# Kernel tuning notes

Hardware: AMD Instinct MI355X
Metric: run time of the kernel (lower is better)

Reference implementation:

```python
import jax, jax.numpy as jnp
import numpy as np

N_NODES = 50000
N_EDGES = 800000
N_FEAT = 256
HIDDEN = 64
N_CLASSES = 16
T_END = 3.0  # opt['time']; rk4 takes one step over [0, 3]


def spline_conv(x, src, dst, p, W, R, b, n):
    """SplineConv, dim=1, kernel_size=2, degree=1 open B-spline, aggr='mean'.
    x: [n, Cin]; src/dst: [E]; p: [E,1] pseudo-coords in [0,1];
    W: [2, Cin, Cout]; R: [Cin, Cout]; b: [Cout]."""
    xj = x[src]  # gather source node features [E, Cin]
    # basis weights for K=2, degree=1: (1-p) on kernel 0, p on kernel 1
    msg = ((1.0 - p) * xj) @ W[0] + (p * xj) @ W[1]  # [E, Cout]
    agg = jax.ops.segment_sum(msg, dst, num_segments=n)
    deg = jax.ops.segment_sum(jnp.ones((msg.shape[0], 1), msg.dtype), dst, num_segments=n)
    return agg / jnp.maximum(deg, 1.0) + x @ R + b


def setup_inputs() -> dict:
    key = jax.random.key(0)
    ks = jax.random.split(key, 20)
    x = jax.random.normal(ks[0], (N_NODES, N_FEAT), jnp.float32)
    edge_attr = jax.random.uniform(ks[1], (N_EDGES, 1), jnp.float32)
    src = jax.random.randint(ks[2], (N_EDGES,), 0, N_NODES)
    dst = jax.random.randint(ks[3], (N_EDGES,), 0, N_NODES)

    def w(k, shape, fan_in):
        s = 1.0 / np.sqrt(fan_in)
        return jax.random.uniform(k, shape, jnp.float32, -s, s)

    # conv1: num_features -> hidden
    W1 = w(ks[4], (2, N_FEAT, HIDDEN), N_FEAT)
    R1 = w(ks[5], (N_FEAT, HIDDEN), N_FEAT)
    b1 = jnp.zeros((HIDDEN,), jnp.float32)
    # ODE func: two stacked SplineConvs hidden -> hidden
    Wa = w(ks[6], (2, HIDDEN, HIDDEN), HIDDEN)
    Ra = w(ks[7], (HIDDEN, HIDDEN), HIDDEN)
    ba = jnp.zeros((HIDDEN,), jnp.float32)
    Wb = w(ks[8], (2, HIDDEN, HIDDEN), HIDDEN)
    Rb = w(ks[9], (HIDDEN, HIDDEN), HIDDEN)
    bb = jnp.zeros((HIDDEN,), jnp.float32)
    # conv2: hidden -> num_classes
    W2 = w(ks[10], (2, HIDDEN, N_CLASSES), HIDDEN)
    R2 = w(ks[11], (HIDDEN, N_CLASSES), HIDDEN)
    b2 = jnp.zeros((N_CLASSES,), jnp.float32)

    return dict(x=x, edge_attr=edge_attr, src=src, dst=dst,
                W1=W1, R1=R1, b1=b1, Wa=Wa, Ra=Ra, ba=ba,
                Wb=Wb, Rb=Rb, bb=bb, W2=W2, R2=R2, b2=b2)


def reference(x, edge_attr, src, dst, W1, R1, b1, Wa, Ra, ba, Wb, Rb, bb, W2, R2, b2):
    n = x.shape[0]
    p = edge_attr
    h = jnp.tanh(spline_conv(x, src, dst, p, W1, R1, b1, n))
    # dropout is identity in eval mode

    def f(y):  # GCNLayer: two stacked SplineConvs, no activation
        y = spline_conv(y, src, dst, p, Wa, Ra, ba, n)
        return spline_conv(y, src, dst, p, Wb, Rb, bb, n)

    # single RK4 step from t=0 to t=T_END (torchdiffeq fixed-grid rk4 on s_span=[0,3])
    k1 = f(h)
    k2 = f(h + 0.5 * T_END * k1)
    k3 = f(h + 0.5 * T_END * k2)
    k4 = f(h + T_END * k3)
    h = h + (T_END / 6.0) * (k1 + 2.0 * k2 + 2.0 * k3 + k4)

    out = jnp.tanh(spline_conv(h, src, dst, p, W2, R2, b2, n))
    return jax.nn.log_softmax(out, axis=1)
```

## Files before the change

### kernel.cpp

```cpp
#include <hip/hip_runtime.h>
#include <math.h>

static inline int ceil_div(int a, int b) { return (a + b - 1) / b; }


__global__ __launch_bounds__(256) void setup_zero_pack(
    int* __restrict__ deg, int* __restrict__ fill, int n,
    const float* __restrict__ W1, const float* __restrict__ R1,
    const float* __restrict__ Wa, const float* __restrict__ Ra,
    const float* __restrict__ Wb, const float* __restrict__ Rb,
    const float* __restrict__ W2, const float* __restrict__ R2,
    float* __restrict__ Bc1, float* __restrict__ Bca,
    float* __restrict__ Bcb, float* __restrict__ Bc2) {
    int gid = blockIdx.x * 256 + threadIdx.x;
    int gstride = gridDim.x * 256;
    for (int i = gid; i < n; i += gstride) { deg[i] = 0; fill[i] = 0; }
    const int S1 = 256 * 192, S2 = 192 * 64, S4 = 64 * 48;
    const int TOT = S1 + 2 * S2 + S4;
    for (int i0 = gid; i0 < TOT; i0 += gstride) {
        int idx = i0;
        if (idx < S1) {
            int k = idx / 192, c = idx % 192;
            float v;
            if (c < 64)       v = W1[k * 64 + c];
            else if (c < 128) v = W1[256 * 64 + k * 64 + (c - 64)];
            else              v = R1[k * 64 + (c - 128)];
            Bc1[idx] = v;
            continue;
        }
        idx -= S1;
        if (idx < S2) { Bca[idx] = (idx < 8192) ? Wa[idx] : Ra[idx - 8192]; continue; }
        idx -= S2;
        if (idx < S2) { Bcb[idx] = (idx < 8192) ? Wb[idx] : Rb[idx - 8192]; continue; }
        idx -= S2;
        int k = idx / 48, c = idx % 48;
        float v;
        if (c < 16)      v = W2[k * 16 + c];
        else if (c < 32) v = W2[64 * 16 + k * 16 + (c - 16)];
        else             v = R2[k * 16 + (c - 32)];
        Bc2[idx] = v;
    }
}

__global__ __launch_bounds__(256) void hist_kernel(const int* __restrict__ dst,
                                                   int* __restrict__ deg, int E) {
    int e = blockIdx.x * 256 + threadIdx.x;
    if (e < E) atomicAdd(&deg[dst[e]], 1);
}

__global__ __launch_bounds__(256) void scan_blocksum(const int* __restrict__ deg,
                                                     int* __restrict__ bsum, int n) {
    __shared__ int red[256];
    int t = threadIdx.x;
    int base = blockIdx.x * 2048 + t * 8;
    int s = 0;
    #pragma unroll
    for (int i = 0; i < 8; ++i) {
        int idx = base + i;
        if (idx < n) s += deg[idx];
    }
    red[t] = s;
    __syncthreads();
    #pragma unroll
    for (int off = 128; off >= 1; off >>= 1) {
        if (t < off) red[t] += red[t + off];
        __syncthreads();
    }
    if (t == 0) bsum[blockIdx.x] = red[0];
}

__global__ __launch_bounds__(256) void scan_tops(int* __restrict__ bsum, int nb) {
    __shared__ int sh[256];
    int t = threadIdx.x;
    int orig = (t < nb) ? bsum[t] : 0;
    sh[t] = orig;
    __syncthreads();
    for (int off = 1; off < 256; off <<= 1) {
        int add = (t >= off) ? sh[t - off] : 0;
        __syncthreads();
        sh[t] += add;
        __syncthreads();
    }
    if (t < nb) bsum[t] = sh[t] - orig;
}

__global__ __launch_bounds__(256) void scan_final(const int* __restrict__ deg,
                                                  const int* __restrict__ bsum,
                                                  int* __restrict__ rowp,
                                                  float* __restrict__ invd,
                                                  int n, int E) {
    __shared__ int sh[256];
    int t = threadIdx.x;
    int base = blockIdx.x * 2048 + t * 8;
    int loc[8];
    int s = 0;
    #pragma unroll
    for (int i = 0; i < 8; ++i) {
        int idx = base + i;
        int d = (idx < n) ? deg[idx] : 0;
        loc[i] = d;
        s += d;
    }
    sh[t] = s;
    __syncthreads();
    for (int off = 1; off < 256; off <<= 1) {
        int add = (t >= off) ? sh[t - off] : 0;
        __syncthreads();
        sh[t] += add;
        __syncthreads();
    }
    int run = bsum[blockIdx.x] + (sh[t] - s);
    #pragma unroll
    for (int i = 0; i < 8; ++i) {
        int idx = base + i;
        if (idx < n) {
            rowp[idx] = run;
            int d = loc[i];
            run += d;
            invd[idx] = 1.0f / (float)(d > 1 ? d : 1);
        }
    }
    if (blockIdx.x == 0 && t == 0) rowp[n] = E;
}

__global__ __launch_bounds__(256) void scatter_idx(const int* __restrict__ dst,
                                                   const int* __restrict__ rowp,
                                                   int* __restrict__ fill,
                                                   int* __restrict__ ei, int E) {
    int e = blockIdx.x * 256 + threadIdx.x;
    if (e >= E) return;
    int d = dst[e];
    int pos = rowp[d] + atomicAdd(&fill[d], 1);
    ei[pos] = e;
}

__global__ __launch_bounds__(256) void sort_fill(const int* __restrict__ rowp,
                                                 int* __restrict__ ei,
                                                 const int* __restrict__ src,
                                                 const float* __restrict__ p,
                                                 int* __restrict__ es,
                                                 float* __restrict__ ep, int n) {
    int node = blockIdx.x * 256 + threadIdx.x;
    if (node >= n) return;
    int b = rowp[node], e = rowp[node + 1];
    for (int i = b + 1; i < e; ++i) {
        int key = ei[i];
        int j = i - 1;
        while (j >= b && ei[j] > key) { ei[j + 1] = ei[j]; --j; }
        ei[j + 1] = key;
    }
    for (int i = b; i < e; ++i) {
        int id = ei[i];
        es[i] = src[id];
        ep[i] = p[id];
    }
}

__global__ __launch_bounds__(256) void edge_agg64_v4(const float* __restrict__ x,
                                                     const int* __restrict__ rowp,
                                                     const int* __restrict__ es,
                                                     const float* __restrict__ ep,
                                                     const float* __restrict__ invd,
                                                     float* __restrict__ agg, int n) {
    int gid = blockIdx.x * 256 + threadIdx.x;
    int node = gid >> 4;
    if (node >= n) return;
    int c4 = (gid & 15) << 2;
    int e = rowp[node], eend = rowp[node + 1];
    float sx = 0.f, sy = 0.f, sz = 0.f, sw = 0.f;
    float px = 0.f, py = 0.f, pz = 0.f, pw = 0.f;
    for (; e + 4 <= eend; e += 4) {
        int s0 = es[e], s1 = es[e + 1], s2 = es[e + 2], s3 = es[e + 3];
        float p0 = ep[e], p1 = ep[e + 1], p2 = ep[e + 2], p3 = ep[e + 3];
        float4 v0 = *reinterpret_cast<const float4*>(&x[(size_t)s0 * 64 + c4]);
        float4 v1 = *reinterpret_cast<const float4*>(&x[(size_t)s1 * 64 + c4]);
        float4 v2 = *reinterpret_cast<const float4*>(&x[(size_t)s2 * 64 + c4]);
        float4 v3 = *reinterpret_cast<const float4*>(&x[(size_t)s3 * 64 + c4]);
        sx += (v0.x + v1.x) + (v2.x + v3.x);
        sy += (v0.y + v1.y) + (v2.y + v3.y);
        sz += (v0.z + v1.z) + (v2.z + v3.z);
        sw += (v0.w + v1.w) + (v2.w + v3.w);
        px = fmaf(p0, v0.x, fmaf(p1, v1.x, fmaf(p2, v2.x, fmaf(p3, v3.x, px))));
        py = fmaf(p0, v0.y, fmaf(p1, v1.y, fmaf(p2, v2.y, fmaf(p3, v3.y, py))));
        pz = fmaf(p0, v0.z, fmaf(p1, v1.z, fmaf(p2, v2.z, fmaf(p3, v3.z, pz))));
        pw = fmaf(p0, v0.w, fmaf(p1, v1.w, fmaf(p2, v2.w, fmaf(p3, v3.w, pw))));
    }
    for (; e < eend; ++e) {
        int s = es[e];
        float pe = ep[e];
        float4 v = *reinterpret_cast<const float4*>(&x[(size_t)s * 64 + c4]);
        sx += v.x; sy += v.y; sz += v.z; sw += v.w;
        px = fmaf(pe, v.x, px); py = fmaf(pe, v.y, py);
        pz = fmaf(pe, v.z, pz); pw = fmaf(pe, v.w, pw);
    }
    float w = invd[node];
    float4 a0 = make_float4((sx - px) * w, (sy - py) * w, (sz - pz) * w, (sw - pw) * w);
    float4 a1 = make_float4(px * w, py * w, pz * w, pw * w);
    *reinterpret_cast<float4*>(&agg[(size_t)node * 128 + c4]) = a0;
    *reinterpret_cast<float4*>(&agg[(size_t)node * 128 + 64 + c4]) = a1;
}

__global__ __launch_bounds__(256) void hidden_gemm_h(
    const float* __restrict__ agg, const float* __restrict__ in,
    const float* __restrict__ B, const float* __restrict__ bias,
    int n, int mode, float* __restrict__ u_out,
    const float* __restrict__ hbuf, const float* __restrict__ acc_in,
    float* __restrict__ acc_out, float* __restrict__ t_out,
    float c1, float c2, float c3) {
    __shared__ __align__(16) float As[2][16][68];
    const int t = threadIdx.x;
    const int row0 = blockIdx.x * 64;
    const int ty = t >> 4, tx = t & 15;
    const int lrow = t >> 2, lk = (t & 3) << 2;

    float4 av = make_float4(0.f, 0.f, 0.f, 0.f);
    {
        int r = row0 + lrow;
        if (r < n) av = *reinterpret_cast<const float4*>(&agg[(size_t)r * 128 + lk]);
    }
    As[0][lk + 0][lrow] = av.x; As[0][lk + 1][lrow] = av.y;
    As[0][lk + 2][lrow] = av.z; As[0][lk + 3][lrow] = av.w;
    __syncthreads();

    float acc[4][4];
    #pragma unroll
    for (int i = 0; i < 4; ++i)
        #pragma unroll
        for (int j = 0; j < 4; ++j) acc[i][j] = 0.f;

    for (int kt = 0; kt < 12; ++kt) {
        const int cur = kt & 1;
        if (kt + 1 < 12) {
            int k0 = (kt + 1) << 4;
            int r = row0 + lrow;
            int kk = k0 + lk;
            av = make_float4(0.f, 0.f, 0.f, 0.f);
            if (r < n)
                av = (kk < 128)
                    ? *reinterpret_cast<const float4*>(&agg[(size_t)r * 128 + kk])
                    : *reinterpret_cast<const float4*>(&in[(size_t)r * 64 + (kk - 128)]);
        }
        const int k0c = kt << 4;
        #pragma unroll
        for (int kk = 0; kk < 16; ++kk) {
            float4 a4 = *reinterpret_cast<const float4*>(&As[cur][kk][ty << 2]);
            float4 b4 = *reinterpret_cast<const float4*>(&B[(size_t)(k0c + kk) * 64 + (tx << 2)]);
            float aa[4] = {a4.x, a4.y, a4.z, a4.w};
            float bb[4] = {b4.x, b4.y, b4.z, b4.w};
            #pragma unroll
            for (int i = 0; i < 4; ++i)
                #pragma unroll
                for (int j = 0; j < 4; ++j)
                    acc[i][j] = fmaf(aa[i], bb[j], acc[i][j]);
        }
        if (kt + 1 < 12) {
            const int nx = cur ^ 1;
            As[nx][lk + 0][lrow] = av.x; As[nx][lk + 1][lrow] = av.y;
            As[nx][lk + 2][lrow] = av.z; As[nx][lk + 3][lrow] = av.w;
        }
        __syncthreads();
    }

    float4 bia = *reinterpret_cast<const float4*>(&bias[tx << 2]);
    #pragma unroll
    for (int i = 0; i < 4; ++i) {
        int r = row0 + (ty << 2) + i;
        if (r >= n) continue;
        size_t idx = (size_t)r * 64 + (tx << 2);
        float4 v = make_float4(acc[i][0] + bia.x, acc[i][1] + bia.y,
                               acc[i][2] + bia.z, acc[i][3] + bia.w);
        if (mode == 0) {
            *reinterpret_cast<float4*>(&u_out[idx]) = v;
        } else {
            float4 ai = make_float4(0.f, 0.f, 0.f, 0.f);
            if (acc_in) ai = *reinterpret_cast<const float4*>(&acc_in[idx]);
            float4 an = make_float4(ai.x + c3 * v.x, ai.y + c3 * v.y,
                                    ai.z + c3 * v.z, ai.w + c3 * v.w);
            *reinterpret_cast<float4*>(&acc_out[idx]) = an;
            float4 hb = *reinterpret_cast<const float4*>(&hbuf[idx]);
            float4 to = make_float4(hb.x + c1 * v.x + c2 * an.x,
                                    hb.y + c1 * v.y + c2 * an.y,
                                    hb.z + c1 * v.z + c2 * an.z,
                                    hb.w + c1 * v.w + c2 * an.w);
            *reinterpret_cast<float4*>(&t_out[idx]) = to;
        }
    }
}

__global__ __launch_bounds__(256) void conv1_gemm_h(const float* __restrict__ x,
                                                    const float* __restrict__ B,
                                                    int n, float* __restrict__ yz,
                                                    float* __restrict__ base,
                                                    const float* __restrict__ b1) {
    __shared__ __align__(16) float As[16][68];
    const int t = threadIdx.x;
    const int row0 = blockIdx.x * 64;
    const int ty = t >> 4, tx = t & 15;
    const int lrow = t >> 2, lk = (t & 3) << 2;
    float acc[4][12];
    #pragma unroll
    for (int i = 0; i < 4; ++i)
        #pragma unroll
        for (int j = 0; j < 12; ++j) acc[i][j] = 0.f;

    for (int kt = 0; kt < 16; ++kt) {
        int k0 = kt << 4;
        float4 av = make_float4(0.f, 0.f, 0.f, 0.f);
        int r = row0 + lrow;
        if (r < n) av = *reinterpret_cast<const float4*>(&x[(size_t)r * 256 + k0 + lk]);
        As[lk + 0][lrow] = av.x; As[lk + 1][lrow] = av.y;
        As[lk + 2][lrow] = av.z; As[lk + 3][lrow] = av.w;
        __syncthreads();
        #pragma unroll
        for (int kk = 0; kk < 16; ++kk) {
            float4 a4 = *reinterpret_cast<const float4*>(&As[kk][ty << 2]);
            const float* bp = &B[(size_t)(k0 + kk) * 192 + (tx << 2)];
            float4 b0 = *reinterpret_cast<const float4*>(bp);
            float4 b1v = *reinterpret_cast<const float4*>(bp + 64);
            float4 b2v = *reinterpret_cast<const float4*>(bp + 128);
            float aa[4] = {a4.x, a4.y, a4.z, a4.w};
            float bb[12] = {b0.x, b0.y, b0.z, b0.w, b1v.x, b1v.y, b1v.z, b1v.w,
                            b2v.x, b2v.y, b2v.z, b2v.w};
            #pragma unroll
            for (int i = 0; i < 4; ++i)
                #pragma unroll
                for (int j = 0; j < 12; ++j)
                    acc[i][j] = fmaf(aa[i], bb[j], acc[i][j]);
        }
        __syncthreads();
    }

    float4 bb4 = *reinterpret_cast<const float4*>(&b1[tx << 2]);
    #pragma unroll
    for (int i = 0; i < 4; ++i) {
        int r = row0 + (ty << 2) + i;
        if (r >= n) continue;
        float4 q0 = make_float4(acc[i][0], acc[i][1], acc[i][2], acc[i][3]);
        float4 q1 = make_float4(acc[i][4], acc[i][5], acc[i][6], acc[i][7]);
        float4 q2 = make_float4(acc[i][8] + bb4.x, acc[i][9] + bb4.y,
                                acc[i][10] + bb4.z, acc[i][11] + bb4.w);
        *reinterpret_cast<float4*>(&yz[(size_t)r * 128 + (tx << 2)]) = q0;
        *reinterpret_cast<float4*>(&yz[(size_t)r * 128 + 64 + (tx << 2)]) = q1;
        *reinterpret_cast<float4*>(&base[(size_t)r * 64 + (tx << 2)]) = q2;
    }
}

__global__ __launch_bounds__(256) void edge_tf64_v8(const float* __restrict__ yz,
                                                    const int* __restrict__ rowp,
                                                    const int* __restrict__ es,
                                                    const float* __restrict__ ep,
                                                    const float* __restrict__ invd,
                                                    const float* __restrict__ base,
                                                    float* __restrict__ out, int n) {
    int gid = blockIdx.x * 256 + threadIdx.x;
    int node = gid >> 3;
    if (node >= n) return;
    int c8 = (gid & 7) << 3;
    int e = rowp[node], eend = rowp[node + 1];
    float a[8] = {0.f, 0.f, 0.f, 0.f, 0.f, 0.f, 0.f, 0.f};
    for (; e + 2 <= eend; e += 2) {
        int s0 = es[e], s1 = es[e + 1];
        float p0 = ep[e], p1 = ep[e + 1];
        float4 y0a = *reinterpret_cast<const float4*>(&yz[(size_t)s0 * 128 + c8]);
        float4 y0b = *reinterpret_cast<const float4*>(&yz[(size_t)s0 * 128 + c8 + 4]);
        float4 z0a = *reinterpret_cast<const float4*>(&yz[(size_t)s0 * 128 + 64 + c8]);
        float4 z0b = *reinterpret_cast<const float4*>(&yz[(size_t)s0 * 128 + 64 + c8 + 4]);
        float4 y1a = *reinterpret_cast<const float4*>(&yz[(size_t)s1 * 128 + c8]);
        float4 y1b = *reinterpret_cast<const float4*>(&yz[(size_t)s1 * 128 + c8 + 4]);
        float4 z1a = *reinterpret_cast<const float4*>(&yz[(size_t)s1 * 128 + 64 + c8]);
        float4 z1b = *reinterpret_cast<const float4*>(&yz[(size_t)s1 * 128 + 64 + c8 + 4]);
        const float* ya0 = &y0a.x; const float* yb0 = &y0b.x;
        const float* za0 = &z0a.x; const float* zb0 = &z0b.x;
        const float* ya1 = &y1a.x; const float* yb1 = &y1b.x;
        const float* za1 = &z1a.x; const float* zb1 = &z1b.x;
        #pragma unroll
        for (int j = 0; j < 4; ++j) {
            a[j]     += fmaf(p0, za0[j] - ya0[j], ya0[j]) + fmaf(p1, za1[j] - ya1[j], ya1[j]);
            a[4 + j] += fmaf(p0, zb0[j] - yb0[j], yb0[j]) + fmaf(p1, zb1[j] - yb1[j], yb1[j]);
        }
    }
    for (; e < eend; ++e) {
        int s = es[e];
        float pe = ep[e];
        float4 ya = *reinterpret_cast<const float4*>(&yz[(size_t)s * 128 + c8]);
        float4 yb = *reinterpret_cast<const float4*>(&yz[(size_t)s * 128 + c8 + 4]);
        float4 za = *reinterpret_cast<const float4*>(&yz[(size_t)s * 128 + 64 + c8]);
        float4 zb = *reinterpret_cast<const float4*>(&yz[(size_t)s * 128 + 64 + c8 + 4]);
        const float* fy = &ya.x; const float* gy = &yb.x;
        const float* fz = &za.x; const float* gz = &zb.x;
        #pragma unroll
        for (int j = 0; j < 4; ++j) {
            a[j]     += fmaf(pe, fz[j] - fy[j], fy[j]);
            a[4 + j] += fmaf(pe, gz[j] - gy[j], gy[j]);
        }
    }
    float w = invd[node];
    size_t idx = (size_t)node * 64 + c8;
    float4 ba = *reinterpret_cast<const float4*>(&base[idx]);
    float4 bbv = *reinterpret_cast<const float4*>(&base[idx + 4]);
    float4 o0 = make_float4(tanhf(fmaf(a[0], w, ba.x)), tanhf(fmaf(a[1], w, ba.y)),
                            tanhf(fmaf(a[2], w, ba.z)), tanhf(fmaf(a[3], w, ba.w)));
    float4 o1 = make_float4(tanhf(fmaf(a[4], w, bbv.x)), tanhf(fmaf(a[5], w, bbv.y)),
                            tanhf(fmaf(a[6], w, bbv.z)), tanhf(fmaf(a[7], w, bbv.w)));
    *reinterpret_cast<float4*>(&out[idx]) = o0;
    *reinterpret_cast<float4*>(&out[idx + 4]) = o1;
}

__global__ __launch_bounds__(256) void edge_tf16_lsm(const float* __restrict__ yz,
                                                     const int* __restrict__ rowp,
                                                     const int* __restrict__ es,
                                                     const float* __restrict__ ep,
                                                     const float* __restrict__ invd,
                                                     const float* __restrict__ base,
                                                     float* __restrict__ out, int n) {
    int gid = blockIdx.x * 256 + threadIdx.x;
    int node = gid >> 4;
    if (node >= n) return;
    int c = gid & 15;
    int e = rowp[node], eend = rowp[node + 1];
    float a = 0.f;
    for (; e + 4 <= eend; e += 4) {
        int s0 = es[e], s1 = es[e + 1], s2 = es[e + 2], s3 = es[e + 3];
        float p0 = ep[e], p1 = ep[e + 1], p2 = ep[e + 2], p3 = ep[e + 3];
        float y0 = yz[(size_t)s0 * 32 + c],      z0 = yz[(size_t)s0 * 32 + 16 + c];
        float y1 = yz[(size_t)s1 * 32 + c],      z1 = yz[(size_t)s1 * 32 + 16 + c];
        float y2 = yz[(size_t)s2 * 32 + c],      z2 = yz[(size_t)s2 * 32 + 16 + c];
        float y3 = yz[(size_t)s3 * 32 + c],      z3 = yz[(size_t)s3 * 32 + 16 + c];
        a += fmaf(p0, z0 - y0, y0);
        a += fmaf(p1, z1 - y1, y1);
        a += fmaf(p2, z2 - y2, y2);
        a += fmaf(p3, z3 - y3, y3);
    }
    for (; e < eend; ++e) {
        int s = es[e]; float pe = ep[e];
        float y = yz[(size_t)s * 32 + c], z = yz[(size_t)s * 32 + 16 + c];
        a += fmaf(pe, z - y, y);
    }
    float o = tanhf(a * invd[node] + base[(size_t)node * 16 + c]);
    float m = o;
    #pragma unroll
    for (int off = 8; off >= 1; off >>= 1) m = fmaxf(m, __shfl_xor(m, off, 16));
    float ex = expf(o - m);
    float s = ex;
    #pragma unroll
    for (int off = 8; off >= 1; off >>= 1) s += __shfl_xor(s, off, 16);
    out[(size_t)node * 16 + c] = (o - m) - logf(s);
}

__global__ __launch_bounds__(256) void conv2_gemm_h(const float* __restrict__ A,
                                                    const float* __restrict__ B,
                                                    int n,
                                                    float* __restrict__ yz2,
                                                    float* __restrict__ base2,
                                                    const float* __restrict__ b2) {
    __shared__ __align__(16) float As[16][68];
    const int t = threadIdx.x;
    const int row0 = blockIdx.x * 64;
    const int ty = t >> 4, tx = t & 15;
    const int lrow = t >> 2, lk = (t & 3) << 2;
    float acc[4][4];
    #pragma unroll
    for (int i = 0; i < 4; ++i)
        #pragma unroll
        for (int j = 0; j < 4; ++j) acc[i][j] = 0.f;

    const bool active = (tx < 12);
    for (int kt = 0; kt < 4; ++kt) {
        int k0 = kt << 4;
        float4 av = make_float4(0.f, 0.f, 0.f, 0.f);
        int r = row0 + lrow;
        if (r < n) av = *reinterpret_cast<const float4*>(&A[(size_t)r * 64 + k0 + lk]);
        As[lk + 0][lrow] = av.x; As[lk + 1][lrow] = av.y;
        As[lk + 2][lrow] = av.z; As[lk + 3][lrow] = av.w;
        __syncthreads();
        if (active) {
            #pragma unroll
            for (int kk = 0; kk < 16; ++kk) {
                float4 a4 = *reinterpret_cast<const float4*>(&As[kk][ty << 2]);
                float4 b4 = *reinterpret_cast<const float4*>(&B[(size_t)(k0 + kk) * 48 + (tx << 2)]);
                float aa[4] = {a4.x, a4.y, a4.z, a4.w};
                float bb[4] = {b4.x, b4.y, b4.z, b4.w};
                #pragma unroll
                for (int i = 0; i < 4; ++i)
                    #pragma unroll
                    for (int j = 0; j < 4; ++j)
                        acc[i][j] = fmaf(aa[i], bb[j], acc[i][j]);
            }
        }
        __syncthreads();
    }

    if (active) {
        #pragma unroll
        for (int i = 0; i < 4; ++i) {
            int r = row0 + (ty << 2) + i;
            if (r >= n) continue;
            #pragma unroll
            for (int j = 0; j < 4; ++j) {
                int c = (tx << 2) + j;
                float v = acc[i][j];
                if (c < 32) yz2[(size_t)r * 32 + c] = v;
                else        base2[(size_t)r * 16 + (c - 32)] = v + b2[c - 32];
            }
        }
    }
}


static void hidden_conv(hipStream_t stream, const float* in, float* agg,
                        const int* rowp, const int* es, const float* ep,
                        const float* invd, const float* Bc, const float* bias, int n,
                        int mode, float* u_out,
                        const float* h, const float* acc_in, float* acc_out,
                        float* t_out, float c1, float c2, float c3) {
    edge_agg64_v4<<<ceil_div(n * 16, 256), 256, 0, stream>>>(in, rowp, es, ep, invd,
                                                             agg, n);
    hidden_gemm_h<<<ceil_div(n, 64), 256, 0, stream>>>(agg, in, Bc, bias, n, mode,
                                                       u_out, h, acc_in, acc_out,
                                                       t_out, c1, c2, c3);
}

extern "C" void kernel_launch(void* const* d_in, const int* in_sizes, int n_in,
                              void* d_out, int out_size, void* d_ws, size_t ws_size,
                              hipStream_t stream) {
    const float* x  = (const float*)d_in[0];
    const float* pE = (const float*)d_in[1];
    const int*   sr = (const int*)d_in[2];
    const int*   ds = (const int*)d_in[3];
    const float* W1 = (const float*)d_in[4];
    const float* R1 = (const float*)d_in[5];
    const float* b1 = (const float*)d_in[6];
    const float* Wa = (const float*)d_in[7];
    const float* Ra = (const float*)d_in[8];
    const float* ba = (const float*)d_in[9];
    const float* Wb = (const float*)d_in[10];
    const float* Rb = (const float*)d_in[11];
    const float* bb = (const float*)d_in[12];
    const float* W2 = (const float*)d_in[13];
    const float* R2 = (const float*)d_in[14];
    const float* b2 = (const float*)d_in[15];
    const int n = in_sizes[0] / 256;
    const int E = in_sizes[2];
    float* out = (float*)d_out;

    char* w = (char*)d_ws;
    auto alloc = [&](size_t bytes) -> void* {
        void* ptr = (void*)w;
        w += (bytes + 255) & ~(size_t)255;
        return ptr;
    };
    int nscan = ceil_div(n, 2048);
    int*   deg  = (int*)alloc((size_t)n * 4);
    int*   fill = (int*)alloc((size_t)n * 4);
    int*   rowp = (int*)alloc((size_t)(n + 1) * 4);
    float* invd = (float*)alloc((size_t)n * 4);
    int*   bsum = (int*)alloc((size_t)256 * 4);
    int*   ei   = (int*)alloc((size_t)E * 4);
    int*   es   = (int*)alloc((size_t)E * 4);
    float* ep   = (float*)alloc((size_t)E * 4);
    float* Bc1  = (float*)alloc((size_t)256 * 192 * 4);
    float* Bca  = (float*)alloc((size_t)192 * 64 * 4);
    float* Bcb  = (float*)alloc((size_t)192 * 64 * 4);
    float* Bc2  = (float*)alloc((size_t)64 * 48 * 4);
    float* big0 = (float*)alloc((size_t)n * 128 * 4);
    float* big1 = (float*)alloc((size_t)n * 64 * 4);
    float* h    = (float*)alloc((size_t)n * 64 * 4);
    float* u    = (float*)alloc((size_t)n * 64 * 4);
    float* tb   = (float*)alloc((size_t)n * 64 * 4);
    float* acc  = (float*)alloc((size_t)n * 64 * 4);

    setup_zero_pack<<<288, 256, 0, stream>>>(deg, fill, n, W1, R1, Wa, Ra, Wb, Rb,
                                             W2, R2, Bc1, Bca, Bcb, Bc2);
    hist_kernel<<<ceil_div(E, 256), 256, 0, stream>>>(ds, deg, E);
    scan_blocksum<<<nscan, 256, 0, stream>>>(deg, bsum, n);
    scan_tops<<<1, 256, 0, stream>>>(bsum, nscan);
    scan_final<<<nscan, 256, 0, stream>>>(deg, bsum, rowp, invd, n, E);
    scatter_idx<<<ceil_div(E, 256), 256, 0, stream>>>(ds, rowp, fill, ei, E);
    sort_fill<<<ceil_div(n, 256), 256, 0, stream>>>(rowp, ei, sr, pE, es, ep, n);

    conv1_gemm_h<<<ceil_div(n, 64), 256, 0, stream>>>(x, Bc1, n, big0, big1, b1);
    edge_tf64_v8<<<ceil_div(n * 8, 256), 256, 0, stream>>>(big0, rowp, es, ep, invd,
                                                           big1, h, n);

    hidden_conv(stream, h, big0, rowp, es, ep, invd, Bca, ba, n, 0, u,
                nullptr, nullptr, nullptr, nullptr, 0.f, 0.f, 0.f);
    hidden_conv(stream, u, big0, rowp, es, ep, invd, Bcb, bb, n, 1, nullptr,
                h, nullptr, acc, tb, 1.5f, 0.f, 1.f);
    hidden_conv(stream, tb, big0, rowp, es, ep, invd, Bca, ba, n, 0, u,
                nullptr, nullptr, nullptr, nullptr, 0.f, 0.f, 0.f);
    hidden_conv(stream, u, big0, rowp, es, ep, invd, Bcb, bb, n, 1, nullptr,
                h, acc, acc, tb, 1.5f, 0.f, 2.f);
    hidden_conv(stream, tb, big0, rowp, es, ep, invd, Bca, ba, n, 0, u,
                nullptr, nullptr, nullptr, nullptr, 0.f, 0.f, 0.f);
    hidden_conv(stream, u, big0, rowp, es, ep, invd, Bcb, bb, n, 1, nullptr,
                h, acc, acc, tb, 3.f, 0.f, 2.f);
    hidden_conv(stream, tb, big0, rowp, es, ep, invd, Bca, ba, n, 0, u,
                nullptr, nullptr, nullptr, nullptr, 0.f, 0.f, 0.f);
    hidden_conv(stream, u, big0, rowp, es, ep, invd, Bcb, bb, n, 1, nullptr,
                h, acc, acc, tb, 0.f, 0.5f, 1.f);

    conv2_gemm_h<<<ceil_div(n, 64), 256, 0, stream>>>(tb, Bc2, n, big0, big1, b2);
    edge_tf16_lsm<<<ceil_div(n * 16, 256), 256, 0, stream>>>(big0, rowp, es, ep, invd,
                                                             big1, out, n);
}
```

Measured before the change: 986.5 us.

## Remap GEMM threads to one row per lane with wave-uniform scalar weight loads

The three dense GEMM kernels (conv1, hidden, conv2) now assign one output row per lane and a contiguous column slice per wavefront, instead of 4x4 register tiles. The column offset is made wave-uniform with readfirstlane, so weight reads can become scalar loads shared across the wave, and each A value is read once per k from LDS. The aim is less vector memory and LDS traffic for the small weight matrices and no idle threads in conv2. The cost is that output stores become row-strided per lane, so they coalesce less well.

```diff
diff --git a/kernel.cpp b/kernel.cpp
--- a/kernel.cpp
+++ b/kernel.cpp
@@ -200,17 +200,18 @@
     *reinterpret_cast<float4*>(&agg[(size_t)node * 128 + 64 + c4]) = a1;
 }
 
-__global__ __launch_bounds__(256) void hidden_gemm_h(
+__global__ __launch_bounds__(256) void hidden_gemm_s(
     const float* __restrict__ agg, const float* __restrict__ in,
     const float* __restrict__ B, const float* __restrict__ bias,
     int n, int mode, float* __restrict__ u_out,
     const float* __restrict__ hbuf, const float* __restrict__ acc_in,
     float* __restrict__ acc_out, float* __restrict__ t_out,
     float c1, float c2, float c3) {
-    __shared__ __align__(16) float As[2][16][68];
+    __shared__ __align__(16) float As[2][16][66];
     const int t = threadIdx.x;
     const int row0 = blockIdx.x * 64;
-    const int ty = t >> 4, tx = t & 15;
+    const int lane = t & 63;
+    const int c0 = __builtin_amdgcn_readfirstlane(t >> 6) << 4;
     const int lrow = t >> 2, lk = (t & 3) << 2;
 
     float4 av = make_float4(0.f, 0.f, 0.f, 0.f);
@@ -222,11 +223,9 @@
     As[0][lk + 2][lrow] = av.z; As[0][lk + 3][lrow] = av.w;
     __syncthreads();
 
-    float acc[4][4];
-    #pragma unroll
-    for (int i = 0; i < 4; ++i)
-        #pragma unroll
-        for (int j = 0; j < 4; ++j) acc[i][j] = 0.f;
+    float acc[16];
+    #pragma unroll
+    for (int j = 0; j < 16; ++j) acc[j] = 0.f;
 
     for (int kt = 0; kt < 12; ++kt) {
         const int cur = kt & 1;
@@ -243,15 +242,11 @@
         const int k0c = kt << 4;
         #pragma unroll
         for (int kk = 0; kk < 16; ++kk) {
-            float4 a4 = *reinterpret_cast<const float4*>(&As[cur][kk][ty << 2]);
-            float4 b4 = *reinterpret_cast<const float4*>(&B[(size_t)(k0c + kk) * 64 + (tx << 2)]);
-            float aa[4] = {a4.x, a4.y, a4.z, a4.w};
-            float bb[4] = {b4.x, b4.y, b4.z, b4.w};
+            float a = As[cur][kk][lane];
+            const float* bp = &B[(size_t)(k0c + kk) * 64 + c0];
             #pragma unroll
-            for (int i = 0; i < 4; ++i)
-                #pragma unroll
-                for (int j = 0; j < 4; ++j)
-                    acc[i][j] = fmaf(aa[i], bb[j], acc[i][j]);
+            for (int j = 0; j < 16; ++j)
+                acc[j] = fmaf(a, bp[j], acc[j]);
         }
         if (kt + 1 < 12) {
             const int nx = cur ^ 1;
@@ -261,14 +256,15 @@
         __syncthreads();
     }
 
-    float4 bia = *reinterpret_cast<const float4*>(&bias[tx << 2]);
-    #pragma unroll
-    for (int i = 0; i < 4; ++i) {
-        int r = row0 + (ty << 2) + i;
-        if (r >= n) continue;
-        size_t idx = (size_t)r * 64 + (tx << 2);
-        float4 v = make_float4(acc[i][0] + bia.x, acc[i][1] + bia.y,
-                               acc[i][2] + bia.z, acc[i][3] + bia.w);
+    int r = row0 + lane;
+    if (r >= n) return;
+    #pragma unroll
+    for (int j4 = 0; j4 < 4; ++j4) {
+        int c = c0 + (j4 << 2);
+        size_t idx = (size_t)r * 64 + c;
+        float4 bia = *reinterpret_cast<const float4*>(&bias[c]);
+        float4 v = make_float4(acc[j4 * 4 + 0] + bia.x, acc[j4 * 4 + 1] + bia.y,
+                               acc[j4 * 4 + 2] + bia.z, acc[j4 * 4 + 3] + bia.w);
         if (mode == 0) {
             *reinterpret_cast<float4*>(&u_out[idx]) = v;
         } else {
@@ -287,21 +283,20 @@
     }
 }
 
-__global__ __launch_bounds__(256) void conv1_gemm_h(const float* __restrict__ x,
+__global__ __launch_bounds__(256) void conv1_gemm_s(const float* __restrict__ x,
                                                     const float* __restrict__ B,
                                                     int n, float* __restrict__ yz,
                                                     float* __restrict__ base,
                                                     const float* __restrict__ b1) {
-    __shared__ __align__(16) float As[16][68];
+    __shared__ __align__(16) float As[16][66];
     const int t = threadIdx.x;
     const int row0 = blockIdx.x * 64;
-    const int ty = t >> 4, tx = t & 15;
+    const int lane = t & 63;
+    const int c0 = __builtin_amdgcn_readfirstlane(t >> 6) * 48;
     const int lrow = t >> 2, lk = (t & 3) << 2;
-    float acc[4][12];
-    #pragma unroll
-    for (int i = 0; i < 4; ++i)
-        #pragma unroll
-        for (int j = 0; j < 12; ++j) acc[i][j] = 0.f;
+    float acc[48];
+    #pragma unroll
+    for (int j = 0; j < 48; ++j) acc[j] = 0.f;
 
     for (int kt = 0; kt < 16; ++kt) {
         int k0 = kt << 4;
@@ -313,37 +308,88 @@
         __syncthreads();
         #pragma unroll
         for (int kk = 0; kk < 16; ++kk) {
-            float4 a4 = *reinterpret_cast<const float4*>(&As[kk][ty << 2]);
-            const float* bp = &B[(size_t)(k0 + kk) * 192 + (tx << 2)];
-            float4 b0 = *reinterpret_cast<const float4*>(bp);
-            float4 b1v = *reinterpret_cast<const float4*>(bp + 64);
-            float4 b2v = *reinterpret_cast<const float4*>(bp + 128);
-            float aa[4] = {a4.x, a4.y, a4.z, a4.w};
-            float bb[12] = {b0.x, b0.y, b0.z, b0.w, b1v.x, b1v.y, b1v.z, b1v.w,
-                            b2v.x, b2v.y, b2v.z, b2v.w};
+            float a = As[kk][lane];
+            const float* bp = &B[(size_t)(k0 + kk) * 192 + c0];
             #pragma unroll
-            for (int i = 0; i < 4; ++i)
+            for (int cg = 0; cg < 3; ++cg)
                 #pragma unroll
-                for (int j = 0; j < 12; ++j)
-                    acc[i][j] = fmaf(aa[i], bb[j], acc[i][j]);
-        }
-        __syncthreads();
-    }
-
-    float4 bb4 = *reinterpret_cast<const float4*>(&b1[tx << 2]);
-    #pragma unroll
-    for (int i = 0; i < 4; ++i) {
-        int r = row0 + (ty << 2) + i;
-        if (r >= n) continue;
-        float4 q0 = make_float4(acc[i][0], acc[i][1], acc[i][2], acc[i][3]);
-        float4 q1 = make_float4(acc[i][4], acc[i][5], acc[i][6], acc[i][7]);
-        float4 q2 = make_float4(acc[i][8] + bb4.x, acc[i][9] + bb4.y,
-                                acc[i][10] + bb4.z, acc[i][11] + bb4.w);
-        *reinterpret_cast<float4*>(&yz[(size_t)r * 128 + (tx << 2)]) = q0;
-        *reinterpret_cast<float4*>(&yz[(size_t)r * 128 + 64 + (tx << 2)]) = q1;
-        *reinterpret_cast<float4*>(&base[(size_t)r * 64 + (tx << 2)]) = q2;
-    }
-}
+                for (int j = 0; j < 16; ++j)
+                    acc[cg * 16 + j] = fmaf(a, bp[cg * 16 + j], acc[cg * 16 + j]);
+        }
+        __syncthreads();
+    }
+
+    int r = row0 + lane;
+    if (r >= n) return;
+    #pragma unroll
+    for (int j4 = 0; j4 < 12; ++j4) {
+        int c = c0 + (j4 << 2);
+        float4 v = make_float4(acc[j4 * 4 + 0], acc[j4 * 4 + 1],
+                               acc[j4 * 4 + 2], acc[j4 * 4 + 3]);
+        if (c < 128) {
+            *reinterpret_cast<float4*>(&yz[(size_t)r * 128 + c]) = v;
+        } else {
+            int cc = c - 128;
+            float4 bia = *reinterpret_cast<const float4*>(&b1[cc]);
+            v.x += bia.x; v.y += bia.y; v.z += bia.z; v.w += bia.w;
+            *reinterpret_cast<float4*>(&base[(size_t)r * 64 + cc]) = v;
+        }
+    }
+}
+
+__global__ __launch_bounds__(256) void conv2_gemm_s(const float* __restrict__ A,
+                                                    const float* __restrict__ B,
+                                                    int n,
+                                                    float* __restrict__ yz2,
+                                                    float* __restrict__ base2,
+                                                    const float* __restrict__ b2) {
+    __shared__ __align__(16) float As[16][66];
+    const int t = threadIdx.x;
+    const int row0 = blockIdx.x * 64;
+    const int lane = t & 63;
+    const int c0 = __builtin_amdgcn_readfirstlane(t >> 6) * 12;
+    const int lrow = t >> 2, lk = (t & 3) << 2;
+    float acc[12];
+    #pragma unroll
+    for (int j = 0; j < 12; ++j) acc[j] = 0.f;
+
+    for (int kt = 0; kt < 4; ++kt) {
+        int k0 = kt << 4;
+        float4 av = make_float4(0.f, 0.f, 0.f, 0.f);
+        int r = row0 + lrow;
+        if (r < n) av = *reinterpret_cast<const float4*>(&A[(size_t)r * 64 + k0 + lk]);
+        As[lk + 0][lrow] = av.x; As[lk + 1][lrow] = av.y;
+        As[lk + 2][lrow] = av.z; As[lk + 3][lrow] = av.w;
+        __syncthreads();
+        #pragma unroll
+        for (int kk = 0; kk < 16; ++kk) {
+            float a = As[kk][lane];
+            const float* bp = &B[(size_t)(k0 + kk) * 48 + c0];
+            #pragma unroll
+            for (int j = 0; j < 12; ++j)
+                acc[j] = fmaf(a, bp[j], acc[j]);
+        }
+        __syncthreads();
+    }
+
+    int r = row0 + lane;
+    if (r >= n) return;
+    #pragma unroll
+    for (int j4 = 0; j4 < 3; ++j4) {
+        int c = c0 + (j4 << 2);
+        float4 v = make_float4(acc[j4 * 4 + 0], acc[j4 * 4 + 1],
+                               acc[j4 * 4 + 2], acc[j4 * 4 + 3]);
+        if (c < 32) {
+            *reinterpret_cast<float4*>(&yz2[(size_t)r * 32 + c]) = v;
+        } else {
+            int cc = c - 32;
+            float4 bia = *reinterpret_cast<const float4*>(&b2[cc]);
+            v.x += bia.x; v.y += bia.y; v.z += bia.z; v.w += bia.w;
+            *reinterpret_cast<float4*>(&base2[(size_t)r * 16 + cc]) = v;
+        }
+    }
+}
+
 
 __global__ __launch_bounds__(256) void edge_tf64_v8(const float* __restrict__ yz,
                                                     const int* __restrict__ rowp,
@@ -447,65 +493,6 @@
     out[(size_t)node * 16 + c] = (o - m) - logf(s);
 }
 
-__global__ __launch_bounds__(256) void conv2_gemm_h(const float* __restrict__ A,
-                                                    const float* __restrict__ B,
-                                                    int n,
-                                                    float* __restrict__ yz2,
-                                                    float* __restrict__ base2,
-                                                    const float* __restrict__ b2) {
-    __shared__ __align__(16) float As[16][68];
-    const int t = threadIdx.x;
-    const int row0 = blockIdx.x * 64;
-    const int ty = t >> 4, tx = t & 15;
-    const int lrow = t >> 2, lk = (t & 3) << 2;
-    float acc[4][4];
-    #pragma unroll
-    for (int i = 0; i < 4; ++i)
-        #pragma unroll
-        for (int j = 0; j < 4; ++j) acc[i][j] = 0.f;
-
-    const bool active = (tx < 12);
-    for (int kt = 0; kt < 4; ++kt) {
-        int k0 = kt << 4;
-        float4 av = make_float4(0.f, 0.f, 0.f, 0.f);
-        int r = row0 + lrow;
-        if (r < n) av = *reinterpret_cast<const float4*>(&A[(size_t)r * 64 + k0 + lk]);
-        As[lk + 0][lrow] = av.x; As[lk + 1][lrow] = av.y;
-        As[lk + 2][lrow] = av.z; As[lk + 3][lrow] = av.w;
-        __syncthreads();
-        if (active) {
-            #pragma unroll
-            for (int kk = 0; kk < 16; ++kk) {
-                float4 a4 = *reinterpret_cast<const float4*>(&As[kk][ty << 2]);
-                float4 b4 = *reinterpret_cast<const float4*>(&B[(size_t)(k0 + kk) * 48 + (tx << 2)]);
-                float aa[4] = {a4.x, a4.y, a4.z, a4.w};
-                float bb[4] = {b4.x, b4.y, b4.z, b4.w};
-                #pragma unroll
-                for (int i = 0; i < 4; ++i)
-                    #pragma unroll
-                    for (int j = 0; j < 4; ++j)
-                        acc[i][j] = fmaf(aa[i], bb[j], acc[i][j]);
-            }
-        }
-        __syncthreads();
-    }
-
-    if (active) {
-        #pragma unroll
-        for (int i = 0; i < 4; ++i) {
-            int r = row0 + (ty << 2) + i;
-            if (r >= n) continue;
-            #pragma unroll
-            for (int j = 0; j < 4; ++j) {
-                int c = (tx << 2) + j;
-                float v = acc[i][j];
-                if (c < 32) yz2[(size_t)r * 32 + c] = v;
-                else        base2[(size_t)r * 16 + (c - 32)] = v + b2[c - 32];
-            }
-        }
-    }
-}
-
 
 static void hidden_conv(hipStream_t stream, const float* in, float* agg,
                         const int* rowp, const int* es, const float* ep,
@@ -515,7 +502,7 @@
                         float* t_out, float c1, float c2, float c3) {
     edge_agg64_v4<<<ceil_div(n * 16, 256), 256, 0, stream>>>(in, rowp, es, ep, invd,
                                                              agg, n);
-    hidden_gemm_h<<<ceil_div(n, 64), 256, 0, stream>>>(agg, in, Bc, bias, n, mode,
+    hidden_gemm_s<<<ceil_div(n, 64), 256, 0, stream>>>(agg, in, Bc, bias, n, mode,
                                                        u_out, h, acc_in, acc_out,
                                                        t_out, c1, c2, c3);
 }
@@ -578,7 +565,7 @@
     scatter_idx<<<ceil_div(E, 256), 256, 0, stream>>>(ds, rowp, fill, ei, E);
     sort_fill<<<ceil_div(n, 256), 256, 0, stream>>>(rowp, ei, sr, pE, es, ep, n);
 
-    conv1_gemm_h<<<ceil_div(n, 64), 256, 0, stream>>>(x, Bc1, n, big0, big1, b1);
+    conv1_gemm_s<<<ceil_div(n, 64), 256, 0, stream>>>(x, Bc1, n, big0, big1, b1);
     edge_tf64_v8<<<ceil_div(n * 8, 256), 256, 0, stream>>>(big0, rowp, es, ep, invd,
                                                            big1, h, n);
 
@@ -599,7 +586,7 @@
     hidden_conv(stream, u, big0, rowp, es, ep, invd, Bcb, bb, n, 1, nullptr,
                 h, acc, acc, tb, 0.f, 0.5f, 1.f);
 
-    conv2_gemm_h<<<ceil_div(n, 64), 256, 0, stream>>>(tb, Bc2, n, big0, big1, b2);
+    conv2_gemm_s<<<ceil_div(n, 64), 256, 0, stream>>>(tb, Bc2, n, big0, big1, b2);
     edge_tf16_lsm<<<ceil_div(n * 16, 256), 256, 0, stream>>>(big0, rowp, es, ep, invd,
                                                              big1, out, n);
 }
```

Result: no change. 0.9997 ms (+1.3%).
